# Performance work log

Hardware: AMD Instinct MI355X
Metric: run time of the kernel (lower is better)

Reference implementation:

```python
import jax, jax.numpy as jnp
import numpy as np

B, T, NA, H, C = 64, 128, 2048, 1024, 10  # batch, time, n_act, hidden_units, classes
FORGET_BIAS = 1.0  # tf BasicLSTMCell default


def setup_inputs() -> dict:
    key = jax.random.key(0)
    ks = jax.random.split(key, 5)
    s = 0.02
    return {
        "inputs": jax.random.normal(ks[0], (B, T, NA), jnp.float32),
        "W0": jax.random.normal(ks[1], (NA + H, 4 * H), jnp.float32) * s,
        "b0": jnp.zeros((4 * H,), jnp.float32),
        "W1": jax.random.normal(ks[2], (2 * H, 4 * H), jnp.float32) * s,
        "b1": jnp.zeros((4 * H,), jnp.float32),
        "Wout": jax.random.normal(ks[3], (H, C), jnp.float32) * s,
        "bout": jnp.zeros((C,), jnp.float32),
    }


def _lstm_step(c, h, x, W, b):
    # tf.contrib.rnn.BasicLSTMCell: z = [x; h] @ W + b, gates order i, j, f, o
    z = jnp.concatenate([x, h], axis=-1) @ W + b
    i, j, f, o = jnp.split(z, 4, axis=-1)
    c_new = c * jax.nn.sigmoid(f + FORGET_BIAS) + jax.nn.sigmoid(i) * jnp.tanh(j)
    h_new = jnp.tanh(c_new) * jax.nn.sigmoid(o)
    return c_new, h_new


def reference(inputs, W0, b0, W1, b1, Wout, bout):
    Bz = inputs.shape[0]
    Hd = Wout.shape[0]

    def step(carry, x_t):
        c0, h0, c1, h1 = carry
        c0, h0 = _lstm_step(c0, h0, x_t, W0, b0)   # layer 0
        c1, h1 = _lstm_step(c1, h1, h0, W1, b1)    # layer 1
        return (c0, h0, c1, h1), h1

    z = jnp.zeros((Bz, Hd), inputs.dtype)
    init = (z, z, z, z)  # zero_state for both layers
    xs = jnp.swapaxes(inputs, 0, 1)  # [T, B, NA]
    _, hs = jax.lax.scan(step, init, xs)  # hs: [T, B, H]
    hs = jnp.swapaxes(hs, 0, 1)  # [B, T, H]
    logits = hs @ Wout + bout  # xw_plus_b on flattened outputs
    preds = jax.nn.softmax(logits, axis=-1)  # [B, T, C]
    return preds
```

## Files before the change

kernel.cpp:

```cpp
#include <hip/hip_runtime.h>
#include <stdint.h>


typedef __attribute__((ext_vector_type(4))) float f32x4;
typedef __attribute__((ext_vector_type(8))) short short8x;
typedef unsigned short ushort_t;

constexpr int B_  = 64;
constexpr int T_  = 128;
constexpr int NA_ = 2048;
constexpr int H_  = 1024;
constexpr int C_  = 10;
constexpr int BT_ = B_ * T_;
constexpr int G4_ = 4 * H_;
constexpr int HB_ = B_ * H_;
constexpr int CH_ = 32;
constexpr int MC_ = B_ * CH_;
constexpr int NWGP_ = 256;

__device__ __forceinline__ ushort_t f2bf(float x) {
    uint32_t u = __float_as_uint(x);
    uint32_t r = (u + 0x7FFFu + ((u >> 16) & 1u)) >> 16;
    return (ushort_t)r;
}
__device__ __forceinline__ float bf2f(ushort_t h) {
    return __uint_as_float((uint32_t)h << 16);
}
__device__ __forceinline__ float sigmf(float x) { return 1.0f / (1.0f + expf(-x)); }

__device__ __forceinline__ void st_u32(void* p, uint32_t v) {
    __hip_atomic_store((uint32_t*)p, v, __ATOMIC_RELAXED, __HIP_MEMORY_SCOPE_AGENT);
}

#define AH_ISSUE(dst, ptr) \
    asm volatile("global_load_dwordx4 %0, %1, off sc0 sc1" : "=v"(dst) : "v"(ptr))

#define GLOAD_LDS(gp, lp) \
    __builtin_amdgcn_global_load_lds((const __attribute__((address_space(1))) uint32_t*)(gp), \
                                     (__attribute__((address_space(3))) uint32_t*)(lp), 16, 0, 0)

__global__ void decomp_chunk(const float* __restrict__ X, int c,
                             ushort_t* __restrict__ Hi, ushort_t* __restrict__ Lo) {
    const int i = blockIdx.x * blockDim.x + threadIdx.x;
    if (i >= MC_ * NA_ / 4) return;
    const int mp = i >> 9;
    const int kq = i & 511;
    const int b = mp >> 5, j = mp & 31;
    const size_t src = ((size_t)(b * T_ + c * CH_ + j)) * NA_ + (size_t)kq * 4;
    float4 v = *(const float4*)(X + src);
    ushort4 hi, lo;
    hi.x = f2bf(v.x); lo.x = f2bf(v.x - bf2f(hi.x));
    hi.y = f2bf(v.y); lo.y = f2bf(v.y - bf2f(hi.y));
    hi.z = f2bf(v.z); lo.z = f2bf(v.z - bf2f(hi.z));
    hi.w = f2bf(v.w); lo.w = f2bf(v.w - bf2f(hi.w));
    ((ushort4*)Hi)[i] = hi;
    ((ushort4*)Lo)[i] = lo;
}

__global__ void transdec(const float* __restrict__ W, int rowOff, int Klen,
                         ushort_t* __restrict__ Thi, ushort_t* __restrict__ Tlo) {
    __shared__ float tile[32][33];
    const int k0 = blockIdx.x * 32, n0 = blockIdx.y * 32;
    const int tx = threadIdx.x & 31, ty = threadIdx.x >> 5;
#pragma unroll
    for (int i = 0; i < 32; i += 8)
        tile[ty + i][tx] = W[(size_t)(rowOff + k0 + ty + i) * G4_ + n0 + tx];
    __syncthreads();
#pragma unroll
    for (int i = 0; i < 32; i += 8) {
        float v = tile[tx][ty + i];
        int n = n0 + ty + i;
        int kk = k0 + tx;
        ushort_t hi = f2bf(v);
        Thi[(size_t)n * Klen + kk] = hi;
        Tlo[(size_t)n * Klen + kk] = f2bf(v - bf2f(hi));
    }
}

__global__ void transb(const float* __restrict__ W, int rowOff, int Klen,
                       ushort_t* __restrict__ Tq) {
    __shared__ float tile[32][33];
    const int k0 = blockIdx.x * 32, n0 = blockIdx.y * 32;
    const int tx = threadIdx.x & 31, ty = threadIdx.x >> 5;
#pragma unroll
    for (int i = 0; i < 32; i += 8)
        tile[ty + i][tx] = W[(size_t)(rowOff + k0 + ty + i) * G4_ + n0 + tx];
    __syncthreads();
#pragma unroll
    for (int i = 0; i < 32; i += 8) {
        float v = tile[tx][ty + i];
        int n = n0 + ty + i;
        Tq[(size_t)n * Klen + k0 + tx] = f2bf(v);
    }
}

__global__ __launch_bounds__(256, 2)
void gemm_bf16x3(const ushort_t* __restrict__ Ahi, const ushort_t* __restrict__ Alo,
                 const ushort_t* __restrict__ Bhi, const ushort_t* __restrict__ Blo,
                 float* __restrict__ C, int M, int N, int K) {
    __shared__ ushort_t sA[2][128 * 64];
    __shared__ ushort_t sB[2][128 * 64];

    const int tid  = threadIdx.x;
    const int lane = tid & 63;
    const int wv   = tid >> 6;
    const int wr   = wv >> 1, wc = wv & 1;
    const int tiles_n = N >> 7;
    int id = blockIdx.x;
    const int q8 = gridDim.x >> 3;
    id = (id & 7) * q8 + (id >> 3);
    const int tm = (id / tiles_n) * 128, tn = (id % tiles_n) * 128;

    f32x4 acc[4][4] = {};

    for (int k0 = 0; k0 < K; k0 += 64) {
#pragma unroll
        for (int rd = 0; rd < 4; ++rd) {
            const int off = rd * 4096 + tid * 16;
            const int r   = off >> 7;
            const int kc  = ((off >> 4) & 7) ^ (r & 7);
            const size_t aoff = (size_t)(tm + r) * K + k0 + kc * 8;
            const size_t boff = (size_t)(tn + r) * K + k0 + kc * 8;
            const int dst = (rd * 4096 + wv * 1024) >> 1;
            GLOAD_LDS(Ahi + aoff, (ushort_t*)sA[0] + dst);
            GLOAD_LDS(Alo + aoff, (ushort_t*)sA[1] + dst);
            GLOAD_LDS(Bhi + boff, (ushort_t*)sB[0] + dst);
            GLOAD_LDS(Blo + boff, (ushort_t*)sB[1] + dst);
        }
        __syncthreads();
#pragma unroll
        for (int ks = 0; ks < 2; ++ks) {
            short8x ah[4], al[4], bh[4], bl[4];
#pragma unroll
            for (int i = 0; i < 4; ++i) {
                const int kc = ks * 4 + (lane >> 4);
                const int ra = wr * 64 + i * 16 + (lane & 15);
                const int ea = ra * 64 + ((kc ^ (ra & 7)) * 8);
                ah[i] = *(const short8x*)(&sA[0][ea]);
                al[i] = *(const short8x*)(&sA[1][ea]);
                const int rb = wc * 64 + i * 16 + (lane & 15);
                const int eb = rb * 64 + ((kc ^ (rb & 7)) * 8);
                bh[i] = *(const short8x*)(&sB[0][eb]);
                bl[i] = *(const short8x*)(&sB[1][eb]);
            }
#pragma unroll
            for (int i = 0; i < 4; ++i)
#pragma unroll
                for (int j = 0; j < 4; ++j) {
                    acc[i][j] = __builtin_amdgcn_mfma_f32_16x16x32_bf16(ah[i], bh[j], acc[i][j], 0, 0, 0);
                    acc[i][j] = __builtin_amdgcn_mfma_f32_16x16x32_bf16(ah[i], bl[j], acc[i][j], 0, 0, 0);
                    acc[i][j] = __builtin_amdgcn_mfma_f32_16x16x32_bf16(al[i], bh[j], acc[i][j], 0, 0, 0);
                }
        }
        __syncthreads();
    }
#pragma unroll
    for (int i = 0; i < 4; ++i)
#pragma unroll
        for (int j = 0; j < 4; ++j)
#pragma unroll
            for (int qq = 0; qq < 4; ++qq) {
                const int row = tm + wr * 64 + i * 16 + (lane >> 4) * 4 + qq;
                const int col = tn + wc * 64 + j * 16 + (lane & 15);
                C[(size_t)row * N + col] = acc[i][j][qq];
            }
}

__device__ __forceinline__ void grid_bar(unsigned* slots, unsigned* flag, unsigned epoch) {
    __syncthreads();
    if (threadIdx.x == 0)
        __hip_atomic_store(&slots[blockIdx.x], epoch, __ATOMIC_RELAXED, __HIP_MEMORY_SCOPE_AGENT);
    if (blockIdx.x == 0) {
        if (threadIdx.x < NWGP_) {
            unsigned spins = 0;
            while (__hip_atomic_load(&slots[threadIdx.x], __ATOMIC_RELAXED, __HIP_MEMORY_SCOPE_AGENT) < epoch
                   && ++spins < (1u << 20))
                __builtin_amdgcn_s_sleep(4);
        }
        __syncthreads();
        if (threadIdx.x == 0)
            __hip_atomic_store(flag, epoch, __ATOMIC_RELAXED, __HIP_MEMORY_SCOPE_AGENT);
    } else {
        if (threadIdx.x == 0) {
            unsigned spins = 0;
            while (__hip_atomic_load(flag, __ATOMIC_RELAXED, __HIP_MEMORY_SCOPE_AGENT) < epoch
                   && ++spins < (1u << 20))
                __builtin_amdgcn_s_sleep(4);
        }
    }
    __syncthreads();
}

__global__ __launch_bounds__(512, 1)
void lstm_persist(int t0, int t1,
                  const float* __restrict__ Z0c,
                  const ushort_t* __restrict__ W0hT, const ushort_t* __restrict__ W1T,
                  const float* __restrict__ b0, const float* __restrict__ b1,
                  ushort_t* __restrict__ h0blk, ushort_t* __restrict__ h1blk,
                  float* __restrict__ c0, float* __restrict__ c1,
                  ushort_t* __restrict__ hsblk, unsigned* slots, unsigned* flag) {
    const int w = blockIdx.x;
    const bool isL0 = (w < 128);
    const int uB = isL0 ? w : (w - 128);
    const int u0 = uB * 8;
    const int tid = threadIdx.x, lane = tid & 63, kv = tid >> 6;
    const int K   = isL0 ? H_ : 2 * H_;
    const int KS  = K >> 3;
    const int NKS = KS >> 5;
    const int kbase = kv * KS;

    __shared__ float zbuf[64][33];

    const ushort_t* Whi = isL0 ? W0hT : W1T;
    short8x wh[2][8] = {};
#pragma unroll
    for (int jn = 0; jn < 2; ++jn)
#pragma unroll
        for (int s = 0; s < 8; ++s)
            if (s < NKS) {
                const int n = jn * 16 + (lane & 15);
                const int grow = (n >> 3) * H_ + u0 + (n & 7);
                wh[jn][s] = *(const short8x*)(Whi + (size_t)grow * K + kbase + s * 32 + (lane >> 4) * 8);
            }

    const bool epi = (tid < 256);
    const int em = tid >> 2;
    const int jp = (tid & 3) * 2;
    const int eu = u0 + jp;
    const float* bias = isL0 ? b0 : b1;
    const float bi0 = epi ? bias[eu]            : 0.f, bi1 = epi ? bias[eu + 1]            : 0.f;
    const float bj0 = epi ? bias[H_ + eu]       : 0.f, bj1 = epi ? bias[H_ + eu + 1]       : 0.f;
    const float bf0 = epi ? bias[2 * H_ + eu]   : 0.f, bf1 = epi ? bias[2 * H_ + eu + 1]   : 0.f;
    const float bo0 = epi ? bias[3 * H_ + eu]   : 0.f, bo1 = epi ? bias[3 * H_ + eu + 1]   : 0.f;
    const int zm = tid >> 3, zj = tid & 7;

    float cr0 = 0.f, cr1 = 0.f;
    float* cptr = (isL0 ? c0 : c1) + (size_t)em * H_ + eu;
    if (epi) { float2 cv = *(const float2*)cptr; cr0 = cv.x; cr1 = cv.y; }

    for (int t = t0; t < t1; ++t) {
        const bool active = isL0 ? (t < T_) : (t >= 1);
        if (active) {
            const int tt = isL0 ? t : t - 1;
            const ushort_t* h0prev = h0blk + ((tt + 1) & 1) * HB_;
            const ushort_t* h0cur  = h0blk + (tt & 1) * HB_;
            const ushort_t* h1prev = h1blk + ((tt + 1) & 1) * HB_;

            zbuf[zm][zj] = 0.f; zbuf[zm][8 + zj] = 0.f;
            zbuf[zm][16 + zj] = 0.f; zbuf[zm][24 + zj] = 0.f;
            __syncthreads();

            float2 zx0 = {0.f, 0.f}, zx1 = {0.f, 0.f}, zx2 = {0.f, 0.f}, zx3 = {0.f, 0.f};
            if (isL0 && epi) {
                const float* zr = Z0c + ((size_t)em * CH_ + (tt & (CH_ - 1))) * G4_;
                zx0 = *(const float2*)(zr + eu);
                zx1 = *(const float2*)(zr + H_ + eu);
                zx2 = *(const float2*)(zr + 2 * H_ + eu);
                zx3 = *(const float2*)(zr + 3 * H_ + eu);
            }

            f32x4 acc[4][2] = {};
            short8x ah[2][4];
            const int npass = NKS >> 1;
#pragma unroll
            for (int pp = 0; pp < 4; ++pp)
                if (pp < npass) {
#pragma unroll
                    for (int s2 = 0; s2 < 2; ++s2) {
                        const int s = pp * 2 + s2;
                        const int kg = kbase + s * 32;
                        const ushort_t* base;
                        int kk;
                        if (isL0)           { base = h0prev; kk = kg; }
                        else if (kg < 1024) { base = h0cur;  kk = kg; }
                        else                { base = h1prev; kk = kg - 1024; }
                        const int kaa = kk + (lane >> 4) * 8;
#pragma unroll
                        for (int i = 0; i < 4; ++i) {
                            const int batch = i * 16 + (lane & 15);
                            AH_ISSUE(ah[s2][i],
                                     base + (size_t)(kaa >> 3) * 512 + (size_t)batch * 8);
                        }
                    }
                    asm volatile("s_waitcnt vmcnt(0)" ::: "memory");
                    __builtin_amdgcn_sched_barrier(0);
#pragma unroll
                    for (int s2 = 0; s2 < 2; ++s2) {
                        const int s = pp * 2 + s2;
#pragma unroll
                        for (int i = 0; i < 4; ++i) {
                            acc[i][0] = __builtin_amdgcn_mfma_f32_16x16x32_bf16(ah[s2][i], wh[0][s], acc[i][0], 0, 0, 0);
                            acc[i][1] = __builtin_amdgcn_mfma_f32_16x16x32_bf16(ah[s2][i], wh[1][s], acc[i][1], 0, 0, 0);
                        }
                    }
                }
#pragma unroll
            for (int i2 = 0; i2 < 4; ++i2) {
                const int i = (i2 + (kv & 3)) & 3;
#pragma unroll
                for (int jn2 = 0; jn2 < 2; ++jn2) {
                    const int jn = (jn2 + (kv >> 2)) & 1;
#pragma unroll
                    for (int qq = 0; qq < 4; ++qq) {
                        const int m = i * 16 + (lane >> 4) * 4 + qq;
                        const int n = jn * 16 + (lane & 15);
                        atomicAdd(&zbuf[m][n], acc[i][jn][qq]);
                    }
                }
            }
            __syncthreads();

            if (epi) {
                const float zi0 = zbuf[em][jp]          + bi0 + zx0.x;
                const float zi1 = zbuf[em][jp + 1]      + bi1 + zx0.y;
                const float zj0 = zbuf[em][8 + jp]      + bj0 + zx1.x;
                const float zj1 = zbuf[em][8 + jp + 1]  + bj1 + zx1.y;
                const float zf0 = zbuf[em][16 + jp]     + bf0 + zx2.x;
                const float zf1 = zbuf[em][16 + jp + 1] + bf1 + zx2.y;
                const float zo0 = zbuf[em][24 + jp]     + bo0 + zx3.x;
                const float zo1 = zbuf[em][24 + jp + 1] + bo1 + zx3.y;
                const float cn0 = cr0 * sigmf(zf0 + 1.0f) + sigmf(zi0) * tanhf(zj0);
                const float cn1 = cr1 * sigmf(zf1 + 1.0f) + sigmf(zi1) * tanhf(zj1);
                cr0 = cn0; cr1 = cn1;
                const float hv0 = tanhf(cn0) * sigmf(zo0);
                const float hv1 = tanhf(cn1) * sigmf(zo1);
                const uint32_t hhp = (uint32_t)f2bf(hv0) | ((uint32_t)f2bf(hv1) << 16);
                const size_t hoff = (size_t)uB * 512 + (size_t)em * 8 + jp;
                if (isL0) {
                    st_u32(h0blk + (tt & 1) * HB_ + hoff, hhp);
                } else {
                    st_u32(h1blk + (tt & 1) * HB_ + hoff, hhp);
                    st_u32(hsblk + ((size_t)tt * 128 + uB) * 512 + (size_t)em * 8 + jp, hhp);
                }
            }
        }
        if (t < T_) grid_bar(slots, flag, (unsigned)(t + 1));
    }

    if (epi) { float2 cv; cv.x = cr0; cv.y = cr1; *(float2*)cptr = cv; }
}

__global__ __launch_bounds__(256)
void out_softmax(const ushort_t* __restrict__ hs, const float* __restrict__ Wout,
                 const float* __restrict__ bout, float* __restrict__ out) {
    const int row  = blockIdx.x * 4 + (threadIdx.x >> 6);
    const int lane = threadIdx.x & 63;
    const int b = row >> 7, t = row & (T_ - 1);
    float s[C_];
#pragma unroll
    for (int c = 0; c < C_; ++c) s[c] = 0.f;
    for (int k = lane; k < H_; k += 64) {
        const float hv = bf2f(hs[((size_t)t * 128 + (k >> 3)) * 512 + (size_t)b * 8 + (k & 7)]);
        const float* w = Wout + k * C_;
#pragma unroll
        for (int c = 0; c < C_; ++c) s[c] += hv * w[c];
    }
#pragma unroll
    for (int c = 0; c < C_; ++c) {
#pragma unroll
        for (int d = 32; d > 0; d >>= 1) s[c] += __shfl_xor(s[c], d);
        s[c] += bout[c];
    }
    float mx = s[0];
#pragma unroll
    for (int c = 1; c < C_; ++c) mx = fmaxf(mx, s[c]);
    float sum = 0.f;
#pragma unroll
    for (int c = 0; c < C_; ++c) { s[c] = expf(s[c] - mx); sum += s[c]; }
    const float inv = 1.0f / sum;
    if (lane < C_) {
        float pv = 0.f;
#pragma unroll
        for (int c = 0; c < C_; ++c)
            if (lane == c) pv = s[c] * inv;
        out[(size_t)row * C_ + lane] = pv;
    }
}

extern "C" void kernel_launch(void* const* d_in, const int* in_sizes, int n_in,
                              void* d_out, int out_size, void* d_ws, size_t ws_size,
                              hipStream_t stream) {
    const float* X    = (const float*)d_in[0];
    const float* W0   = (const float*)d_in[1];
    const float* b0   = (const float*)d_in[2];
    const float* W1   = (const float*)d_in[3];
    const float* b1   = (const float*)d_in[4];
    const float* Wout = (const float*)d_in[5];
    const float* bout = (const float*)d_in[6];
    float* out = (float*)d_out;

    char* p = (char*)d_ws;
    size_t off = 0;
    auto take = [&](size_t bytes) { char* r = p + off; off += bytes; return r; };
    ushort_t* W0xT_hi = (ushort_t*)take((size_t)G4_ * NA_ * 2);
    ushort_t* W0xT_lo = (ushort_t*)take((size_t)G4_ * NA_ * 2);
    ushort_t* W0hT    = (ushort_t*)take((size_t)G4_ * H_ * 2);
    ushort_t* W1T     = (ushort_t*)take((size_t)G4_ * 2 * H_ * 2);
    ushort_t* Xc_hi   = (ushort_t*)take((size_t)MC_ * NA_ * 2);
    ushort_t* Xc_lo   = (ushort_t*)take((size_t)MC_ * NA_ * 2);
    float*    Z0c     = (float*)take((size_t)MC_ * G4_ * 4);
    ushort_t* hsblk   = (ushort_t*)take((size_t)BT_ * H_ * 2);
    float*    c0      = (float*)take((size_t)B_ * H_ * 4);
    float*    c1      = (float*)take((size_t)B_ * H_ * 4);
    ushort_t* h0blk   = (ushort_t*)take((size_t)2 * HB_ * 2);
    ushort_t* h1blk   = (ushort_t*)take((size_t)2 * HB_ * 2);
    unsigned* bar     = (unsigned*)take(2048);
    if (ws_size < off) return;

    unsigned* slots = bar;
    unsigned* flag  = bar + 256;

    (void)hipMemsetAsync(c0, 0, (size_t)B_ * H_ * 4, stream);
    (void)hipMemsetAsync(c1, 0, (size_t)B_ * H_ * 4, stream);
    (void)hipMemsetAsync(h0blk + HB_, 0, (size_t)HB_ * 2, stream);
    (void)hipMemsetAsync(h1blk + HB_, 0, (size_t)HB_ * 2, stream);
    (void)hipMemsetAsync(bar, 0, 2048, stream);

    transdec<<<dim3(NA_ / 32, G4_ / 32), 256, 0, stream>>>(W0, 0, NA_, W0xT_hi, W0xT_lo);
    transb  <<<dim3(H_ / 32, G4_ / 32), 256, 0, stream>>>(W0, NA_, H_, W0hT);
    transb  <<<dim3(2 * H_ / 32, G4_ / 32), 256, 0, stream>>>(W1, 0, 2 * H_, W1T);

    for (int c = 0; c < T_ / CH_; ++c) {
        decomp_chunk<<<(MC_ * NA_ / 4 + 255) / 256, 256, 0, stream>>>(X, c, Xc_hi, Xc_lo);
        gemm_bf16x3<<<(MC_ / 128) * (G4_ / 128), 256, 0, stream>>>(
            Xc_hi, Xc_lo, W0xT_hi, W0xT_lo, Z0c, MC_, G4_, NA_);
        lstm_persist<<<NWGP_, 512, 0, stream>>>(c * CH_, c * CH_ + CH_, Z0c,
                                                W0hT, W1T, b0, b1, h0blk, h1blk,
                                                c0, c1, hsblk, slots, flag);
    }
    lstm_persist<<<NWGP_, 512, 0, stream>>>(T_, T_ + 1, Z0c,
                                            W0hT, W1T, b0, b1, h0blk, h1blk,
                                            c0, c1, hsblk, slots, flag);

    out_softmax<<<BT_ / 4, 256, 0, stream>>>(hsblk, Wout, bout, out);
}
```

Measured before the change: 4.128 ms.

## Retile persistent LSTM workgroups to 16 units by 32 batch rows

Each workgroup now owns 16 hidden units across half the batch (32 rows), where before it owned 8 units across all 64 rows. Per step it loads half as much h activation data from global memory and keeps twice as many weight fragments in registers, so each A fragment feeds four MFMAs instead of two. The LDS reduction buffer, epilogue indexing and h output addressing are rearranged to match. Register pressure rises, since the weight fragments held per thread double.

```diff
diff --git a/kernel.cpp b/kernel.cpp
--- a/kernel.cpp
+++ b/kernel.cpp
@@ -201,38 +201,42 @@
                   ushort_t* __restrict__ hsblk, unsigned* slots, unsigned* flag) {
     const int w = blockIdx.x;
     const bool isL0 = (w < 128);
-    const int uB = isL0 ? w : (w - 128);
-    const int u0 = uB * 8;
+    const int lw = isL0 ? w : (w - 128);
+    const int uB16 = lw >> 1;
+    const int mh   = lw & 1;
+    const int u0 = uB16 * 16;
+    const int m0 = mh * 32;
     const int tid = threadIdx.x, lane = tid & 63, kv = tid >> 6;
     const int K   = isL0 ? H_ : 2 * H_;
     const int KS  = K >> 3;
     const int NKS = KS >> 5;
     const int kbase = kv * KS;
 
-    __shared__ float zbuf[64][33];
+    __shared__ float zbuf[32][65];
 
     const ushort_t* Whi = isL0 ? W0hT : W1T;
-    short8x wh[2][8] = {};
-#pragma unroll
-    for (int jn = 0; jn < 2; ++jn)
+    short8x wh[4][8] = {};
+#pragma unroll
+    for (int jn = 0; jn < 4; ++jn)
 #pragma unroll
         for (int s = 0; s < 8; ++s)
             if (s < NKS) {
                 const int n = jn * 16 + (lane & 15);
-                const int grow = (n >> 3) * H_ + u0 + (n & 7);
+                const int grow = (n >> 4) * H_ + u0 + (n & 15);
                 wh[jn][s] = *(const short8x*)(Whi + (size_t)grow * K + kbase + s * 32 + (lane >> 4) * 8);
             }
 
     const bool epi = (tid < 256);
-    const int em = tid >> 2;
-    const int jp = (tid & 3) * 2;
+    const int ml = tid >> 3;
+    const int em = m0 + ml;
+    const int jp = (tid & 7) * 2;
     const int eu = u0 + jp;
     const float* bias = isL0 ? b0 : b1;
     const float bi0 = epi ? bias[eu]            : 0.f, bi1 = epi ? bias[eu + 1]            : 0.f;
     const float bj0 = epi ? bias[H_ + eu]       : 0.f, bj1 = epi ? bias[H_ + eu + 1]       : 0.f;
     const float bf0 = epi ? bias[2 * H_ + eu]   : 0.f, bf1 = epi ? bias[2 * H_ + eu + 1]   : 0.f;
     const float bo0 = epi ? bias[3 * H_ + eu]   : 0.f, bo1 = epi ? bias[3 * H_ + eu + 1]   : 0.f;
-    const int zm = tid >> 3, zj = tid & 7;
+    const int zm = tid >> 4, zj = (tid & 15) * 4;
 
     float cr0 = 0.f, cr1 = 0.f;
     float* cptr = (isL0 ? c0 : c1) + (size_t)em * H_ + eu;
@@ -246,8 +250,8 @@
             const ushort_t* h0cur  = h0blk + (tt & 1) * HB_;
             const ushort_t* h1prev = h1blk + ((tt + 1) & 1) * HB_;
 
-            zbuf[zm][zj] = 0.f; zbuf[zm][8 + zj] = 0.f;
-            zbuf[zm][16 + zj] = 0.f; zbuf[zm][24 + zj] = 0.f;
+            zbuf[zm][zj] = 0.f; zbuf[zm][zj + 1] = 0.f;
+            zbuf[zm][zj + 2] = 0.f; zbuf[zm][zj + 3] = 0.f;
             __syncthreads();
 
             float2 zx0 = {0.f, 0.f}, zx1 = {0.f, 0.f}, zx2 = {0.f, 0.f}, zx3 = {0.f, 0.f};
@@ -259,8 +263,8 @@
                 zx3 = *(const float2*)(zr + 3 * H_ + eu);
             }
 
-            f32x4 acc[4][2] = {};
-            short8x ah[2][4];
+            f32x4 acc[2][4] = {};
+            short8x ah[2][2];
             const int npass = NKS >> 1;
 #pragma unroll
             for (int pp = 0; pp < 4; ++pp)
@@ -276,8 +280,8 @@
                         else                { base = h1prev; kk = kg - 1024; }
                         const int kaa = kk + (lane >> 4) * 8;
 #pragma unroll
-                        for (int i = 0; i < 4; ++i) {
-                            const int batch = i * 16 + (lane & 15);
+                        for (int i = 0; i < 2; ++i) {
+                            const int batch = m0 + i * 16 + (lane & 15);
                             AH_ISSUE(ah[s2][i],
                                      base + (size_t)(kaa >> 3) * 512 + (size_t)batch * 8);
                         }
@@ -288,18 +292,20 @@
                     for (int s2 = 0; s2 < 2; ++s2) {
                         const int s = pp * 2 + s2;
 #pragma unroll
-                        for (int i = 0; i < 4; ++i) {
+                        for (int i = 0; i < 2; ++i) {
                             acc[i][0] = __builtin_amdgcn_mfma_f32_16x16x32_bf16(ah[s2][i], wh[0][s], acc[i][0], 0, 0, 0);
                             acc[i][1] = __builtin_amdgcn_mfma_f32_16x16x32_bf16(ah[s2][i], wh[1][s], acc[i][1], 0, 0, 0);
+                            acc[i][2] = __builtin_amdgcn_mfma_f32_16x16x32_bf16(ah[s2][i], wh[2][s], acc[i][2], 0, 0, 0);
+                            acc[i][3] = __builtin_amdgcn_mfma_f32_16x16x32_bf16(ah[s2][i], wh[3][s], acc[i][3], 0, 0, 0);
                         }
                     }
                 }
 #pragma unroll
-            for (int i2 = 0; i2 < 4; ++i2) {
-                const int i = (i2 + (kv & 3)) & 3;
-#pragma unroll
-                for (int jn2 = 0; jn2 < 2; ++jn2) {
-                    const int jn = (jn2 + (kv >> 2)) & 1;
+            for (int i2 = 0; i2 < 2; ++i2) {
+                const int i = (i2 + (kv & 1)) & 1;
+#pragma unroll
+                for (int jn2 = 0; jn2 < 4; ++jn2) {
+                    const int jn = (jn2 + (kv >> 1)) & 3;
 #pragma unroll
                     for (int qq = 0; qq < 4; ++qq) {
                         const int m = i * 16 + (lane >> 4) * 4 + qq;
@@ -311,26 +317,27 @@
             __syncthreads();
 
             if (epi) {
-                const float zi0 = zbuf[em][jp]          + bi0 + zx0.x;
-                const float zi1 = zbuf[em][jp + 1]      + bi1 + zx0.y;
-                const float zj0 = zbuf[em][8 + jp]      + bj0 + zx1.x;
-                const float zj1 = zbuf[em][8 + jp + 1]  + bj1 + zx1.y;
-                const float zf0 = zbuf[em][16 + jp]     + bf0 + zx2.x;
-                const float zf1 = zbuf[em][16 + jp + 1] + bf1 + zx2.y;
-                const float zo0 = zbuf[em][24 + jp]     + bo0 + zx3.x;
-                const float zo1 = zbuf[em][24 + jp + 1] + bo1 + zx3.y;
+                const float zi0 = zbuf[ml][jp]          + bi0 + zx0.x;
+                const float zi1 = zbuf[ml][jp + 1]      + bi1 + zx0.y;
+                const float zj0 = zbuf[ml][16 + jp]     + bj0 + zx1.x;
+                const float zj1 = zbuf[ml][16 + jp + 1] + bj1 + zx1.y;
+                const float zf0 = zbuf[ml][32 + jp]     + bf0 + zx2.x;
+                const float zf1 = zbuf[ml][32 + jp + 1] + bf1 + zx2.y;
+                const float zo0 = zbuf[ml][48 + jp]     + bo0 + zx3.x;
+                const float zo1 = zbuf[ml][48 + jp + 1] + bo1 + zx3.y;
                 const float cn0 = cr0 * sigmf(zf0 + 1.0f) + sigmf(zi0) * tanhf(zj0);
                 const float cn1 = cr1 * sigmf(zf1 + 1.0f) + sigmf(zi1) * tanhf(zj1);
                 cr0 = cn0; cr1 = cn1;
                 const float hv0 = tanhf(cn0) * sigmf(zo0);
                 const float hv1 = tanhf(cn1) * sigmf(zo1);
                 const uint32_t hhp = (uint32_t)f2bf(hv0) | ((uint32_t)f2bf(hv1) << 16);
-                const size_t hoff = (size_t)uB * 512 + (size_t)em * 8 + jp;
+                const int kb = uB16 * 2 + (jp >> 3);
+                const size_t hoff = ((size_t)kb * 64 + em) * 8 + (jp & 7);
                 if (isL0) {
                     st_u32(h0blk + (tt & 1) * HB_ + hoff, hhp);
                 } else {
                     st_u32(h1blk + (tt & 1) * HB_ + hoff, hhp);
-                    st_u32(hsblk + ((size_t)tt * 128 + uB) * 512 + (size_t)em * 8 + jp, hhp);
+                    st_u32(hsblk + (((size_t)tt * 128 + kb) * 64 + em) * 8 + (jp & 7), hhp);
                 }
             }
         }
```

Measured after the change: 3.995 ms. 3.2% less time.
